# Kernel optimization log

Measured on AMD Instinct MI355X. Metric: run time of the kernel, lower is better.

Reference implementation:

```python
import jax, jax.numpy as jnp
import numpy as np

LAYERS, BLOCKS = 10, 3
NL = LAYERS * BLOCKS
DC, RC, SC, CLASSES, K = 128, 128, 256, 256, 2
SR = 4096  # number of output samples sliced from the end
N, L, EN = 4, 8192, 16


def _conv1x1(x, w):
    # x: [N, Cin, L], w: [Cout, Cin] -> [N, Cout, L]
    return jnp.einsum('ncl,oc->nol', x, w)


def _condition(x, enc):
    # x: [N, C, L], enc: [N, C, En], L % En == 0; tiled periodic add (faithful to the view trick)
    n, c, l = x.shape
    en = enc.shape[2]
    return (x.reshape(n, c, l // en, en) + enc[:, :, None, :]).reshape(n, c, l)


def _dilated_causal_conv(x, w, d):
    # kernel_size=2 causal dilated conv. x: [N, Cin, L], w: [Cout, Cin, 2]
    xs = jnp.pad(x, ((0, 0), (0, 0), (d, 0)))[:, :, :x.shape[2]]  # x delayed by d
    return jnp.einsum('ncl,oc->nol', xs, w[:, :, 0]) + jnp.einsum('ncl,oc->nol', x, w[:, :, 1])


def setup_inputs() -> dict:
    key = jax.random.key(0)
    ks = jax.random.split(key, 12)
    s = 0.05
    return {
        'x': jax.random.normal(ks[0], (N, CLASSES, L), jnp.float32),
        'en': jax.random.normal(ks[1], (N, CLASSES, EN), jnp.float32),
        'start1_w': jax.random.normal(ks[2], (RC, CLASSES), jnp.float32) * s,
        'start2_w': jax.random.normal(ks[3], (SC, RC), jnp.float32) * s,
        'cond_w': jax.random.normal(ks[4], (NL, 2 * DC, CLASSES), jnp.float32) * s,
        'dil_w': jax.random.normal(ks[5], (NL, 2 * DC, RC, K), jnp.float32) * s,
        'res_w': jax.random.normal(ks[6], (NL, RC, DC), jnp.float32) * s,
        'skip_w': jax.random.normal(ks[7], (NL, SC, DC), jnp.float32) * s,
        'end1_w': jax.random.normal(ks[8], (CLASSES, SC), jnp.float32) * s,
        'end1_b': jnp.zeros((CLASSES,), jnp.float32),
        'end2_w': jax.random.normal(ks[9], (CLASSES, CLASSES), jnp.float32) * s,
        'end2_b': jnp.zeros((CLASSES,), jnp.float32),
    }


def reference(x, en, start1_w, start2_w, cond_w, dil_w, res_w, skip_w,
              end1_w, end1_b, end2_w, end2_b):
    l = _conv1x1(x, start1_w)          # [N, RC, L]
    s = _conv1x1(l, start2_w)          # [N, SC, L]
    for i in range(NL):
        dil = 2 ** (i % LAYERS)
        d = _dilated_causal_conv(l, dil_w[i], dil)      # [N, 2*DC, L]
        d = _condition(d, _conv1x1(en, cond_w[i]))
        g = jax.nn.sigmoid(d[:, :DC]) * jnp.tanh(d[:, DC:])  # gated, [N, DC, L]
        l = l + _conv1x1(g, res_w[i])
        s = s + _conv1x1(g, skip_w[i])
    s = jax.nn.relu(s)
    s = _conv1x1(s, end1_w) + end1_b[None, :, None]
    s = _condition(s, _conv1x1(en, end2_w) + end2_b[None, :, None])
    s = jax.nn.relu(s)
    return s[:, :, -SR:]
```

## Files before the change

### kernel.cpp

```cpp
#include <hip/hip_runtime.h>

typedef __bf16 bf16_t;
typedef __bf16 bf16x8 __attribute__((ext_vector_type(8)));
typedef __bf16 bf16x4 __attribute__((ext_vector_type(4)));
typedef float  f32x4  __attribute__((ext_vector_type(4)));
typedef int    i32x4  __attribute__((ext_vector_type(4)));

#define PL 136
#define PX 264

__device__ __forceinline__ f32x4 mfma16(bf16x8 a, bf16x8 b, f32x4 c) {
    return __builtin_amdgcn_mfma_f32_16x16x32_bf16(a, b, c, 0, 0, 0);
}

__device__ __forceinline__ void conv_elem(const float* __restrict__ src,
                                          bf16_t* __restrict__ dst,
                                          int idx, int M, int K) {
    int MK = M * K;
    int lay = idx / MK;
    int r = idx - lay * MK;
    int j = r & 7, lane = (r >> 3) & 63, rest = r >> 9;
    int KB = K >> 5;
    int kb = rest % KB, mt = rest / KB;
    int m = mt * 16 + (lane & 15);
    int k = kb * 32 + ((lane >> 4) << 3) + j;
    dst[idx] = (bf16_t)src[(size_t)lay * MK + m * K + k];
}

__global__ void k_prep(const float* __restrict__ rw, const float* __restrict__ kw,
                       const float* __restrict__ s1w, const float* __restrict__ s2w,
                       const float* __restrict__ e1w, const float* __restrict__ dwt,
                       const float* __restrict__ cond_w, const float* __restrict__ end2_w,
                       const float* __restrict__ end2_b, const float* __restrict__ en,
                       bf16_t* __restrict__ Ares, bf16_t* __restrict__ Askp,
                       bf16_t* __restrict__ A1, bf16_t* __restrict__ A2,
                       bf16_t* __restrict__ Ae, bf16_t* __restrict__ Adil,
                       float* __restrict__ cond_all, float* __restrict__ cond2) {
    __shared__ f32x4 en_s[1024];
    if (blockIdx.x >= 13952) {
        int bi = blockIdx.x - 13952;
        int i = bi >> 2, n = bi & 3, o = threadIdx.x;
        const f32x4* ep = (const f32x4*)(en + (size_t)n * 4096);
        for (int idx = threadIdx.x; idx < 1024; idx += 256) en_s[idx] = ep[idx];
        __syncthreads();
        const float* W = (i < 30) ? cond_w + ((size_t)i * 256 + o) * 256
                                  : end2_w + (size_t)o * 256;
        f32x4 a0 = {0.f,0.f,0.f,0.f}, a1 = a0, a2 = a0, a3 = a0;
        for (int c = 0; c < 256; c += 4) {
            f32x4 wv = *(const f32x4*)(W + c);
            #pragma unroll
            for (int cc = 0; cc < 4; ++cc) {
                float wf = wv[cc];
                a0 += wf * en_s[(c + cc) * 4 + 0];
                a1 += wf * en_s[(c + cc) * 4 + 1];
                a2 += wf * en_s[(c + cc) * 4 + 2];
                a3 += wf * en_s[(c + cc) * 4 + 3];
            }
        }
        float bias = (i < 30) ? 0.f : end2_b[o];
        float* dst = (i < 30) ? cond_all + (((size_t)i * 4 + n) * 256 + o) * 16
                              : cond2 + ((size_t)n * 256 + o) * 16;
        f32x4* d4 = (f32x4*)dst;
        d4[0] = a0 + bias; d4[1] = a1 + bias; d4[2] = a2 + bias; d4[3] = a3 + bias;
        return;
    }
    int idx = blockIdx.x * 256 + threadIdx.x;
    if (idx < 491520) { conv_elem(rw, Ares, idx, 128, 128); return; }
    idx -= 491520;
    if (idx < 983040) { conv_elem(kw, Askp, idx, 256, 128); return; }
    idx -= 983040;
    if (idx < 32768) { conv_elem(s1w, A1, idx, 128, 256); return; }
    idx -= 32768;
    if (idx < 32768) { conv_elem(s2w, A2, idx, 256, 128); return; }
    idx -= 32768;
    if (idx < 65536) { conv_elem(e1w, Ae, idx, 256, 256); return; }
    idx -= 65536;
    {
        int lay = idx >> 16, r = idx & 65535;
        int j = r & 7, lane = (r >> 3) & 63, rest = r >> 9;
        int kb = rest & 7, mt = rest >> 3;
        int m = mt * 16 + (lane & 15);
        int k = kb * 32 + ((lane >> 4) << 3) + j;
        float v = (k < 128) ? dwt[(((size_t)lay * 256 + m) * 128 + k) * 2]
                            : dwt[(((size_t)lay * 256 + m) * 128 + (k - 128)) * 2 + 1];
        Adil[(size_t)lay * 65536 + r] = (bf16_t)v;
    }
}

__global__ __launch_bounds__(512, 4) void k_start(
    const float* __restrict__ x, bf16_t* __restrict__ la, float* __restrict__ sbuf,
    const bf16_t* __restrict__ A1, const bf16_t* __restrict__ A2, int t_base)
{
    __shared__ __align__(16) bf16_t xt[64 * PX];
    __shared__ __align__(16) bf16_t l0[64 * PL];
    int tid = threadIdx.x;
    int n = blockIdx.y, t0 = t_base + blockIdx.x * 64;
    int lane = tid & 63, w = tid >> 6, i16 = lane & 15, q = lane >> 4;
    f32x4 z = {0.f,0.f,0.f,0.f};
    {
        int t = tid & 63;
        for (int c = tid >> 6; c < 256; c += 8)
            xt[t * PX + c] = (bf16_t)x[((size_t)n * 256 + c) * 8192 + t0 + t];
    }
    __syncthreads();
    f32x4 acc[4] = {z,z,z,z};
    #pragma unroll
    for (int kb = 0; kb < 8; ++kb) {
        int koff = kb * 32 + q * 8;
        bf16x8 bf[4];
        #pragma unroll
        for (int nt = 0; nt < 4; ++nt)
            bf[nt] = *(const bf16x8*)(xt + (nt * 16 + i16) * PX + koff);
        bf16x8 af = *(const bf16x8*)(A1 + (((size_t)w * 8 + kb) * 64 + lane) * 8);
        #pragma unroll
        for (int nt = 0; nt < 4; ++nt) acc[nt] = mfma16(af, bf[nt], acc[nt]);
    }
    #pragma unroll
    for (int nt = 0; nt < 4; ++nt)
        #pragma unroll
        for (int j = 0; j < 4; ++j)
            l0[(nt * 16 + i16) * PL + w * 16 + q * 4 + j] = (bf16_t)acc[nt][j];
    __syncthreads();
    {
        int r = tid >> 4, col = (tid & 15) * 8;
        #pragma unroll
        for (int p = 0; p < 2; ++p) {
            int rr = r + p * 32;
            *(i32x4*)(la + ((size_t)n * 8192 + t0 + rr) * 128 + col) =
                *(const i32x4*)(l0 + rr * PL + col);
        }
    }
    if (t0 >= 4096) {
        f32x4 a2[2][4] = {{z,z,z,z},{z,z,z,z}};
        #pragma unroll
        for (int kb = 0; kb < 4; ++kb) {
            int koff = kb * 32 + q * 8;
            bf16x8 bf[4];
            #pragma unroll
            for (int nt = 0; nt < 4; ++nt)
                bf[nt] = *(const bf16x8*)(l0 + (nt * 16 + i16) * PL + koff);
            #pragma unroll
            for (int mt2 = 0; mt2 < 2; ++mt2) {
                bf16x8 af = *(const bf16x8*)(A2 + ((((size_t)2 * w + mt2) * 4 + kb) * 64 + lane) * 8);
                #pragma unroll
                for (int nt = 0; nt < 4; ++nt) a2[mt2][nt] = mfma16(af, bf[nt], a2[mt2][nt]);
            }
        }
        float* sp = sbuf + (size_t)n * 256 * 4096 + (t0 - 4096);
        #pragma unroll
        for (int mt2 = 0; mt2 < 2; ++mt2)
            #pragma unroll
            for (int nt = 0; nt < 4; ++nt)
                #pragma unroll
                for (int j = 0; j < 4; ++j) {
                    int o = (2 * w + mt2) * 16 + q * 4 + j;
                    sp[(size_t)o * 4096 + nt * 16 + i16] = a2[mt2][nt][j];
                }
    }
}

template<int USEG>
__global__ __launch_bounds__(512, 8) void k_layer(
    const bf16_t* __restrict__ l_in, bf16_t* __restrict__ l_out,
    float* __restrict__ sbuf, bf16_t* __restrict__ Gl,
    const bf16_t* __restrict__ Ad, const bf16_t* __restrict__ Ar,
    const bf16_t* __restrict__ Ak, const float* __restrict__ condL,
    int dil, int t_base, int do_res)
{
    __shared__ __align__(16) bf16_t smA[64 * PL];
    __shared__ __align__(16) bf16_t sm2[32 * PL];
    int tid = threadIdx.x;
    int n = blockIdx.y, t0 = t_base + blockIdx.x * 32;
    int lane = tid & 63, w = tid >> 6, i16 = lane & 15, q = lane >> 4;
    f32x4 z = {0.f,0.f,0.f,0.f};
    const float* cond = condL + (size_t)n * 4096;
    int r = tid >> 4, col = (tid & 15) * 8;
    size_t base = (size_t)n * 8192;
    const bf16_t* curp;
    const bf16_t* delp;
    if (dil < 32) {
        int cnt = (32 + dil) * 16;
        for (int idx = tid; idx < cnt; idx += 512) {
            int rr = idx >> 4, c2 = (idx & 15) * 8;
            *(i32x4*)(smA + rr * PL + c2) =
                *(const i32x4*)(l_in + (base + t0 - dil + rr) * 128 + c2);
        }
        delp = smA; curp = smA + dil * PL;
    } else {
        *(i32x4*)(smA + r * PL + col) =
            *(const i32x4*)(l_in + (base + t0 + r) * 128 + col);
        int gp = t0 - dil + r;
        i32x4 v = {0, 0, 0, 0};
        if (gp >= 0) v = *(const i32x4*)(l_in + (base + gp) * 128 + col);
        *(i32x4*)(smA + (32 + r) * PL + col) = v;
        curp = smA; delp = smA + 32 * PL;
    }
    __syncthreads();

    f32x4 accs[2] = {z,z}, acct[2] = {z,z};
    const bf16x8* AdF = (const bf16x8*)Ad;
    #pragma unroll
    for (int kb = 0; kb < 8; ++kb) {
        const bf16_t* bsrc = (kb < 4) ? delp : curp;
        int koff = (kb & 3) * 32 + q * 8;
        bf16x8 bf[2];
        #pragma unroll
        for (int nt = 0; nt < 2; ++nt)
            bf[nt] = *(const bf16x8*)(bsrc + (nt * 16 + i16) * PL + koff);
        bf16x8 a_s = AdF[((size_t)w * 8 + kb) * 64 + lane];
        bf16x8 a_t = AdF[((size_t)(w + 8) * 8 + kb) * 64 + lane];
        #pragma unroll
        for (int nt = 0; nt < 2; ++nt) {
            accs[nt] = mfma16(a_s, bf[nt], accs[nt]);
            acct[nt] = mfma16(a_t, bf[nt], acct[nt]);
        }
    }
    int c_base = w * 16 + q * 4;
    {
        float cv_s[4], cv_t[4];
        #pragma unroll
        for (int j = 0; j < 4; ++j) {
            cv_s[j] = cond[(c_base + j) * 16 + i16];
            cv_t[j] = cond[(c_base + j + 128) * 16 + i16];
        }
        #pragma unroll
        for (int nt = 0; nt < 2; ++nt) {
            bf16x4 g4;
            #pragma unroll
            for (int j = 0; j < 4; ++j) {
                float vlo = accs[nt][j] + cv_s[j];
                float vhi = acct[nt][j] + cv_t[j];
                float sg = 1.0f / (1.0f + __expf(-vlo));
                float th = 1.0f - 2.0f / (1.0f + __expf(2.0f * vhi));
                g4[j] = (bf16_t)(sg * th);
            }
            *(bf16x4*)(sm2 + (nt * 16 + i16) * PL + c_base) = g4;
        }
    }
    __syncthreads();

    if (USEG) {
        if (t0 >= 4096) {
            bf16_t* gd = Gl + ((size_t)n * 4096 + (t0 - 4096) + r) * 128 + col;
            *(i32x4*)gd = *(const i32x4*)(sm2 + r * PL + col);
        }
    }

    f32x4 acc2[2] = {z,z};
    const bf16x8* ArF = (const bf16x8*)Ar;
    if (do_res || !USEG) {
        int do_skip = (!USEG) && (t0 >= 4096);
        f32x4 acc3[2][2] = {{z,z},{z,z}};
        const bf16x8* AkF = (const bf16x8*)Ak;
        #pragma unroll
        for (int kb = 0; kb < 4; ++kb) {
            int koff = kb * 32 + q * 8;
            bf16x8 bf[2];
            #pragma unroll
            for (int nt = 0; nt < 2; ++nt)
                bf[nt] = *(const bf16x8*)(sm2 + (nt * 16 + i16) * PL + koff);
            if (do_res) {
                bf16x8 ar = ArF[((size_t)w * 4 + kb) * 64 + lane];
                #pragma unroll
                for (int nt = 0; nt < 2; ++nt) acc2[nt] = mfma16(ar, bf[nt], acc2[nt]);
            }
            if (do_skip) {
                #pragma unroll
                for (int mt2 = 0; mt2 < 2; ++mt2) {
                    bf16x8 ak = AkF[((size_t)(2 * w + mt2) * 4 + kb) * 64 + lane];
                    #pragma unroll
                    for (int nt = 0; nt < 2; ++nt)
                        acc3[mt2][nt] = mfma16(ak, bf[nt], acc3[mt2][nt]);
                }
            }
        }
        if (do_skip) {
            float* sp = sbuf + (size_t)n * 256 * 4096 + (t0 - 4096);
            #pragma unroll
            for (int mt2 = 0; mt2 < 2; ++mt2)
                #pragma unroll
                for (int nt = 0; nt < 2; ++nt)
                    #pragma unroll
                    for (int j = 0; j < 4; ++j) {
                        int o = (2 * w + mt2) * 16 + q * 4 + j;
                        sp[(size_t)o * 4096 + nt * 16 + i16] += acc3[mt2][nt][j];
                    }
        }
    }

    if (do_res) {
        bf16x4 o4[2];
        #pragma unroll
        for (int nt = 0; nt < 2; ++nt) {
            int trow = (nt * 16 + i16) * PL;
            bf16x4 lv = *(const bf16x4*)(curp + trow + c_base);
            #pragma unroll
            for (int j = 0; j < 4; ++j)
                o4[nt][j] = (bf16_t)((float)lv[j] + acc2[nt][j]);
        }
        __syncthreads();
        #pragma unroll
        for (int nt = 0; nt < 2; ++nt)
            *(bf16x4*)(sm2 + (nt * 16 + i16) * PL + c_base) = o4[nt];
        __syncthreads();
        bf16_t* dst = l_out + (base + t0 + r) * 128 + col;
        *(i32x4*)dst = *(const i32x4*)(sm2 + r * PL + col);
    }
}

__global__ __launch_bounds__(512, 8) void k_skip(
    const bf16_t* __restrict__ G, float* __restrict__ sbuf,
    const bf16_t* __restrict__ Askp)
{
    __shared__ __align__(16) bf16_t gbuf[2][32 * PL];
    int tid = threadIdx.x;
    int n = blockIdx.y, t0 = blockIdx.x * 32;
    int lane = tid & 63, w = tid >> 6, i16 = lane & 15, q = lane >> 4;
    f32x4 z = {0.f,0.f,0.f,0.f};
    f32x4 acc[2][2] = {{z,z},{z,z}};
    int r = tid >> 4, cA = (tid & 15) * 8;
    const size_t GLS = (size_t)4 * 4096 * 128;
    const bf16_t* gb = G + ((size_t)n * 4096 + t0 + r) * 128 + cA;
    i32x4 v[4];
    #pragma unroll
    for (int d = 0; d < 4; ++d) v[d] = *(const i32x4*)(gb + (size_t)d * GLS);
    #pragma unroll 1
    for (int i = 0; i < 30; ++i) {
        *(i32x4*)(gbuf[i & 1] + r * PL + cA) = v[i & 3];
        if (i + 4 < 30) v[i & 3] = *(const i32x4*)(gb + (size_t)(i + 4) * GLS);
        __syncthreads();
        const bf16x8* AkF = (const bf16x8*)(Askp + (size_t)i * 32768);
        const bf16_t* gB = gbuf[i & 1];
        #pragma unroll
        for (int kb = 0; kb < 4; ++kb) {
            int koff = kb * 32 + q * 8;
            bf16x8 ak0 = AkF[((size_t)(2 * w) * 4 + kb) * 64 + lane];
            bf16x8 ak1 = AkF[((size_t)(2 * w + 1) * 4 + kb) * 64 + lane];
            #pragma unroll
            for (int nt = 0; nt < 2; ++nt) {
                bf16x8 bf = *(const bf16x8*)(gB + (nt * 16 + i16) * PL + koff);
                acc[0][nt] = mfma16(ak0, bf, acc[0][nt]);
                acc[1][nt] = mfma16(ak1, bf, acc[1][nt]);
            }
        }
    }
    float* sp = sbuf + (size_t)n * 256 * 4096 + t0;
    #pragma unroll
    for (int mt2 = 0; mt2 < 2; ++mt2)
        #pragma unroll
        for (int nt = 0; nt < 2; ++nt)
            #pragma unroll
            for (int j = 0; j < 4; ++j) {
                int o = (2 * w + mt2) * 16 + q * 4 + j;
                sp[(size_t)o * 4096 + nt * 16 + i16] += acc[mt2][nt][j];
            }
}

__global__ __launch_bounds__(512) void k_end(
    const float* __restrict__ sbuf, float* __restrict__ out,
    const bf16_t* __restrict__ Ae, const float* __restrict__ cond2,
    const float* __restrict__ b1)
{
    __shared__ __align__(16) bf16_t st[64 * PX];
    __shared__ float c2[4096];
    __shared__ float b1s[256];
    int tid = threadIdx.x;
    int n = blockIdx.y, t0 = blockIdx.x * 64;
    int lane = tid & 63, w = tid >> 6, i16 = lane & 15, q = lane >> 4;
    f32x4 z = {0.f,0.f,0.f,0.f};
    {
        int t = tid & 63;
        for (int c = tid >> 6; c < 256; c += 8) {
            float v = sbuf[((size_t)n * 256 + c) * 4096 + t0 + t];
            st[t * PX + c] = (bf16_t)fmaxf(v, 0.f);
        }
        const f32x4* cc = (const f32x4*)(cond2 + (size_t)n * 4096);
        for (int idx = tid; idx < 1024; idx += 512) ((f32x4*)c2)[idx] = cc[idx];
        if (tid < 64) ((f32x4*)b1s)[tid] = ((const f32x4*)b1)[tid];
    }
    __syncthreads();
    f32x4 acc[2][4] = {{z,z,z,z},{z,z,z,z}};
    #pragma unroll
    for (int kb = 0; kb < 8; ++kb) {
        int koff = kb * 32 + q * 8;
        bf16x8 bf[4];
        #pragma unroll
        for (int nt = 0; nt < 4; ++nt)
            bf[nt] = *(const bf16x8*)(st + (nt * 16 + i16) * PX + koff);
        #pragma unroll
        for (int mt2 = 0; mt2 < 2; ++mt2) {
            bf16x8 af = *(const bf16x8*)(Ae + ((((size_t)2 * w + mt2) * 8 + kb) * 64 + lane) * 8);
            #pragma unroll
            for (int nt = 0; nt < 4; ++nt) acc[mt2][nt] = mfma16(af, bf[nt], acc[mt2][nt]);
        }
    }
    #pragma unroll
    for (int mt2 = 0; mt2 < 2; ++mt2)
        #pragma unroll
        for (int j = 0; j < 4; ++j) {
            int o = (2 * w + mt2) * 16 + q * 4 + j;
            float bb = b1s[o] + c2[o * 16 + i16];
            #pragma unroll
            for (int nt = 0; nt < 4; ++nt) {
                float v = acc[mt2][nt][j] + bb;
                out[((size_t)n * 256 + o) * 4096 + t0 + nt * 16 + i16] = fmaxf(v, 0.f);
            }
        }
}

extern "C" void kernel_launch(void* const* d_in, const int* in_sizes, int n_in,
                              void* d_out, int out_size, void* d_ws, size_t ws_size,
                              hipStream_t stream) {
    const float* x   = (const float*)d_in[0];
    const float* en  = (const float*)d_in[1];
    const float* s1w = (const float*)d_in[2];
    const float* s2w = (const float*)d_in[3];
    const float* cw  = (const float*)d_in[4];
    const float* dw  = (const float*)d_in[5];
    const float* rw  = (const float*)d_in[6];
    const float* kw  = (const float*)d_in[7];
    const float* e1w = (const float*)d_in[8];
    const float* e1b = (const float*)d_in[9];
    const float* e2w = (const float*)d_in[10];
    const float* e2b = (const float*)d_in[11];
    float* out = (float*)d_out;

    char* p = (char*)d_ws;
    auto take = [&](size_t bytes) {
        char* r = p;
        p += (bytes + 255) & ~(size_t)255;
        return r;
    };
    bf16_t* A1   = (bf16_t*)take((size_t)128 * 256 * 2);
    bf16_t* A2   = (bf16_t*)take((size_t)256 * 128 * 2);
    bf16_t* Ae   = (bf16_t*)take((size_t)256 * 256 * 2);
    bf16_t* Adil = (bf16_t*)take((size_t)30 * 65536 * 2);
    bf16_t* Ares = (bf16_t*)take((size_t)30 * 16384 * 2);
    bf16_t* Askp = (bf16_t*)take((size_t)30 * 32768 * 2);
    float*  condA= (float*)take((size_t)30 * 16384 * 4);
    float*  cond2= (float*)take((size_t)16384 * 4);
    bf16_t* la   = (bf16_t*)take((size_t)4 * 8192 * 128 * 2);
    bf16_t* lb   = (bf16_t*)take((size_t)4 * 8192 * 128 * 2);
    float*  sbuf = (float*)take((size_t)4 * 256 * 4096 * 4);
    bf16_t* G    = (bf16_t*)take((size_t)30 * 4 * 4096 * 128 * 2);
    bool useG = ((size_t)(p - (char*)d_ws) <= ws_size);

    k_prep<<<14076, 256, 0, stream>>>(rw, kw, s1w, s2w, e1w, dw,
                                      cw, e2w, e2b, en,
                                      Ares, Askp, A1, A2, Ae, Adil, condA, cond2);

    int a[30];
    a[29] = 4096;
    for (int i = 28; i >= 0; --i) {
        int nx = a[i + 1] - (1 << ((i + 1) % 10));
        a[i] = nx < 4096 ? (nx & ~63) : 4096;
    }

    k_start<<<dim3(127, 4), 512, 0, stream>>>(x, la, sbuf, A1, A2, 64);

    bf16_t* src = la;
    bf16_t* dst = lb;
    for (int i = 0; i < 30; ++i) {
        dim3 grid((8192 - a[i]) / 32, 4);
        if (useG)
            k_layer<1><<<grid, 512, 0, stream>>>(src, dst, sbuf,
                G + (size_t)i * 4 * 4096 * 128,
                Adil + (size_t)i * 65536, Ares + (size_t)i * 16384,
                Askp + (size_t)i * 32768, condA + (size_t)i * 16384,
                1 << (i % 10), a[i], i < 29 ? 1 : 0);
        else
            k_layer<0><<<grid, 512, 0, stream>>>(src, dst, sbuf, (bf16_t*)nullptr,
                Adil + (size_t)i * 65536, Ares + (size_t)i * 16384,
                Askp + (size_t)i * 32768, condA + (size_t)i * 16384,
                1 << (i % 10), a[i], i < 29 ? 1 : 0);
        bf16_t* t = src; src = dst; dst = t;
    }
    if (useG)
        k_skip<<<dim3(128, 4), 512, 0, stream>>>(G, sbuf, Askp);
    k_end<<<dim3(64, 4), 512, 0, stream>>>(sbuf, out, Ae, cond2, e1b);
}
```

Baseline: 629.4 us.

## Store gated activations in MFMA fragment order and widen skip-GEMM tiles

The layer kernel now writes the gated G buffer in the exact per-lane MFMA B-fragment order, so the skip kernel can copy it contiguously into LDS and read fragments with no padding or transposition. The residual output is written straight from registers, dropping one LDS round-trip and two barriers. The skip kernel now processes 64 time steps per block, halving the grid, and uses a restructured double-buffered pipeline with a single barrier per iteration. In exchange it holds more registers per thread and gives less parallelism; the direct residual stores are 8-byte rather than 16-byte coalesced writes.

```diff
diff --git a/kernel.cpp b/kernel.cpp
--- a/kernel.cpp
+++ b/kernel.cpp
@@ -241,8 +241,10 @@
 
     if (USEG) {
         if (t0 >= 4096) {
-            bf16_t* gd = Gl + ((size_t)n * 4096 + (t0 - 4096) + r) * 128 + col;
-            *(i32x4*)gd = *(const i32x4*)(sm2 + r * PL + col);
+            int tt = ((tid & 256) >> 4) + (tid & 15);
+            int cc = ((tid >> 6) & 3) * 32 + ((tid >> 4) & 3) * 8;
+            bf16x8 gv = *(const bf16x8*)(sm2 + tt * PL + cc);
+            *(bf16x8*)(Gl + ((size_t)n * 4096 + (t0 - 4096)) * 128 + tid * 8) = gv;
         }
     }
 
@@ -289,66 +291,78 @@
     }
 
     if (do_res) {
-        bf16x4 o4[2];
         #pragma unroll
         for (int nt = 0; nt < 2; ++nt) {
             int trow = (nt * 16 + i16) * PL;
             bf16x4 lv = *(const bf16x4*)(curp + trow + c_base);
+            bf16x4 o4;
             #pragma unroll
             for (int j = 0; j < 4; ++j)
-                o4[nt][j] = (bf16_t)((float)lv[j] + acc2[nt][j]);
-        }
-        __syncthreads();
-        #pragma unroll
-        for (int nt = 0; nt < 2; ++nt)
-            *(bf16x4*)(sm2 + (nt * 16 + i16) * PL + c_base) = o4[nt];
-        __syncthreads();
-        bf16_t* dst = l_out + (base + t0 + r) * 128 + col;
-        *(i32x4*)dst = *(const i32x4*)(sm2 + r * PL + col);
-    }
-}
-
-__global__ __launch_bounds__(512, 8) void k_skip(
+                o4[j] = (bf16_t)((float)lv[j] + acc2[nt][j]);
+            *(bf16x4*)(l_out + (base + t0 + nt * 16 + i16) * 128 + c_base) = o4;
+        }
+    }
+}
+
+__global__ __launch_bounds__(512, 4) void k_skip(
     const bf16_t* __restrict__ G, float* __restrict__ sbuf,
     const bf16_t* __restrict__ Askp)
 {
-    __shared__ __align__(16) bf16_t gbuf[2][32 * PL];
+    __shared__ __align__(16) bf16_t gbuf[2][8192];
     int tid = threadIdx.x;
-    int n = blockIdx.y, t0 = blockIdx.x * 32;
+    int n = blockIdx.y, t0 = blockIdx.x * 64;
     int lane = tid & 63, w = tid >> 6, i16 = lane & 15, q = lane >> 4;
     f32x4 z = {0.f,0.f,0.f,0.f};
-    f32x4 acc[2][2] = {{z,z},{z,z}};
-    int r = tid >> 4, cA = (tid & 15) * 8;
+    f32x4 acc[2][4] = {{z,z,z,z},{z,z,z,z}};
     const size_t GLS = (size_t)4 * 4096 * 128;
-    const bf16_t* gb = G + ((size_t)n * 4096 + t0 + r) * 128 + cA;
-    i32x4 v[4];
-    #pragma unroll
-    for (int d = 0; d < 4; ++d) v[d] = *(const i32x4*)(gb + (size_t)d * GLS);
+    const bf16_t* gb = G + ((size_t)n * 4096 + t0) * 128 + tid * 8;
+    i32x4 v0[4], v1[4];
+    #pragma unroll
+    for (int d = 0; d < 4; ++d) {
+        v0[d] = *(const i32x4*)(gb + (size_t)d * GLS);
+        v1[d] = *(const i32x4*)(gb + (size_t)d * GLS + 4096);
+    }
+    *(i32x4*)(gbuf[0] + tid * 8) = v0[0];
+    *(i32x4*)(gbuf[0] + 4096 + tid * 8) = v1[0];
+    v0[0] = *(const i32x4*)(gb + (size_t)4 * GLS);
+    v1[0] = *(const i32x4*)(gb + (size_t)4 * GLS + 4096);
+    __syncthreads();
     #pragma unroll 1
     for (int i = 0; i < 30; ++i) {
-        *(i32x4*)(gbuf[i & 1] + r * PL + cA) = v[i & 3];
-        if (i + 4 < 30) v[i & 3] = *(const i32x4*)(gb + (size_t)(i + 4) * GLS);
-        __syncthreads();
         const bf16x8* AkF = (const bf16x8*)(Askp + (size_t)i * 32768);
         const bf16_t* gB = gbuf[i & 1];
         #pragma unroll
         for (int kb = 0; kb < 4; ++kb) {
-            int koff = kb * 32 + q * 8;
             bf16x8 ak0 = AkF[((size_t)(2 * w) * 4 + kb) * 64 + lane];
             bf16x8 ak1 = AkF[((size_t)(2 * w + 1) * 4 + kb) * 64 + lane];
             #pragma unroll
-            for (int nt = 0; nt < 2; ++nt) {
-                bf16x8 bf = *(const bf16x8*)(gB + (nt * 16 + i16) * PL + koff);
+            for (int nt = 0; nt < 4; ++nt) {
+                bf16x8 bf = *(const bf16x8*)(gB + (nt >> 1) * 4096 +
+                                             (((nt & 1) * 4 + kb) * 64 + lane) * 8);
                 acc[0][nt] = mfma16(ak0, bf, acc[0][nt]);
                 acc[1][nt] = mfma16(ak1, bf, acc[1][nt]);
             }
         }
+        if (i + 1 < 30) {
+            int s = (i + 1) & 3;
+            bf16_t* db = gbuf[(i + 1) & 1];
+            *(i32x4*)(db + tid * 8) = v0[s];
+            *(i32x4*)(db + 4096 + tid * 8) = v1[s];
+            if (i + 5 < 30) {
+                v0[s] = *(const i32x4*)(gb + (size_t)(i + 5) * GLS);
+                v1[s] = *(const i32x4*)(gb + (size_t)(i + 5) * GLS + 4096);
+            }
+            asm volatile("s_waitcnt lgkmcnt(0)" ::: "memory");
+            __builtin_amdgcn_sched_barrier(0);
+            __builtin_amdgcn_s_barrier();
+            __builtin_amdgcn_sched_barrier(0);
+        }
     }
     float* sp = sbuf + (size_t)n * 256 * 4096 + t0;
     #pragma unroll
     for (int mt2 = 0; mt2 < 2; ++mt2)
         #pragma unroll
-        for (int nt = 0; nt < 2; ++nt)
+        for (int nt = 0; nt < 4; ++nt)
             #pragma unroll
             for (int j = 0; j < 4; ++j) {
                 int o = (2 * w + mt2) * 16 + q * 4 + j;
@@ -476,6 +490,6 @@
         bf16_t* t = src; src = dst; dst = t;
     }
     if (useG)
-        k_skip<<<dim3(128, 4), 512, 0, stream>>>(G, sbuf, Askp);
+        k_skip<<<dim3(64, 4), 512, 0, stream>>>(G, sbuf, Askp);
     k_end<<<dim3(64, 4), 512, 0, stream>>>(sbuf, out, Ae, cond2, e1b);
 }
```

Result: slower. 647.3 us (+2.8%).
